# Optimization experiments

Hardware: AMD Instinct MI355X
Metric: run time of the kernel (lower is better)

## Reference

```python
import jax, jax.numpy as jnp
import numpy as np

B, N, D = 8, 4096, 256
H = 8
DH = D // H          # 32 per-head dim
M = 256              # number of random features
DEPTH = 4
HID = 4 * D          # mlp hidden
EPS = 1e-6


def layernorm(x, g, b):
    mu = jnp.mean(x, axis=-1, keepdims=True)
    var = jnp.mean(jnp.square(x - mu), axis=-1, keepdims=True)
    return (x - mu) * jax.lax.rsqrt(var + EPS) * g + b


def _phi(t, proj, is_query):
    # t: (B,H,N,DH), proj: (M,DH) -> (B,H,N,M) nonnegative softmax-kernel features
    nrm = DH ** -0.25
    td = t * nrm
    u = jnp.einsum('bhnd,md->bhnm', td, proj)
    diag = 0.5 * jnp.sum(td * td, axis=-1, keepdims=True)
    if is_query:
        mx = jnp.max(u, axis=-1, keepdims=True)
    else:
        mx = jnp.max(u, axis=(-2, -1), keepdims=True)
    return (jnp.exp(u - diag - mx) + 1e-4) / jnp.sqrt(jnp.asarray(M, t.dtype))


def performer_attn(h, Wqkv, Wproj, bproj, proj):
    # h: (B,N,D)
    qkv = h @ Wqkv                                   # (B,N,3D)
    q, k, v = jnp.split(qkv, 3, axis=-1)
    to_heads = lambda t: t.reshape(B, N, H, DH).transpose(0, 2, 1, 3)
    q, k, v = to_heads(q), to_heads(k), to_heads(v)  # (B,H,N,DH)
    qp = _phi(q, proj, True)                         # (B,H,N,M)
    kp = _phi(k, proj, False)                        # (B,H,N,M)
    kv = jnp.einsum('bhnm,bhnd->bhmd', kp, v)        # (B,H,M,DH) linear-time context
    z = 1.0 / (jnp.einsum('bhnm,bhm->bhn', qp, kp.sum(axis=2)) + 1e-6)
    out = jnp.einsum('bhnm,bhmd->bhnd', qp, kv) * z[..., None]
    out = out.transpose(0, 2, 1, 3).reshape(B, N, D)
    return out @ Wproj + bproj


def mlp(h, W1, b1, W2, b2):
    return jax.nn.gelu(h @ W1 + b1, approximate=False) @ W2 + b2


def setup_inputs() -> dict:
    key = jax.random.key(0)
    ks = jax.random.split(key, 10)
    inp = {
        'x': jax.random.normal(ks[0], (B, N, D), jnp.float32),
        'pos_emb': 0.02 * jax.random.normal(ks[1], (N, D), jnp.float32),
        'g1n': jnp.ones((D,), jnp.float32),
        'b1n': jnp.zeros((D,), jnp.float32),
        'g2n': jnp.ones((D,), jnp.float32),
        'b2n': jnp.zeros((D,), jnp.float32),
        'Wqkv': 0.02 * jax.random.normal(ks[2], (DEPTH, D, 3 * D), jnp.float32),
        'Wproj': 0.02 * jax.random.normal(ks[3], (DEPTH, D, D), jnp.float32),
        'bproj': jnp.zeros((DEPTH, D), jnp.float32),
        'W1': 0.02 * jax.random.normal(ks[4], (DEPTH, D, HID), jnp.float32),
        'b1m': jnp.zeros((DEPTH, HID), jnp.float32),
        'W2': 0.02 * jax.random.normal(ks[5], (DEPTH, HID, D), jnp.float32),
        'b2m': jnp.zeros((DEPTH, D), jnp.float32),
        'proj_mat': jax.random.normal(ks[6], (DEPTH, M, DH), jnp.float32),
    }
    return inp


def reference(x, pos_emb, g1n, b1n, g2n, b2n, Wqkv, Wproj, bproj, W1, b1m, W2, b2m, proj_mat):
    h = x + pos_emb[None]
    for l in range(DEPTH):  # small fixed depth
        h = h + performer_attn(layernorm(h, g1n, b1n), Wqkv[l], Wproj[l], bproj[l], proj_mat[l])
        h = h + mlp(layernorm(h, g2n, b2n), W1[l], b1m[l], W2[l], b2m[l])
    return h
```

## Files before the change

### kernel.cpp

```cpp
#include <hip/hip_runtime.h>
#include <hip/hip_bf16.h>
#include <math.h>

#define B 8
#define N 4096
#define D 256
#define H 8
#define DH 32
#define M 256
#define DEPTH 4
#define HID 1024
#define NRM 0.4204482076268573f

typedef __attribute__((ext_vector_type(8))) short short8;
typedef __attribute__((ext_vector_type(4))) float f32x4;

static __device__ __forceinline__ unsigned short f2bf(float f) {
    __hip_bfloat16 h = __float2bfloat16(f);
    return __builtin_bit_cast(unsigned short, h);
}
static __device__ __forceinline__ float bfu2f(unsigned short u) {
    unsigned int x = ((unsigned int)u) << 16;
    return __builtin_bit_cast(float, x);
}

__global__ void add_pos_kernel(const float* __restrict__ x, const float* __restrict__ pos,
                               float* __restrict__ h) {
    int i = blockIdx.x * 256 + threadIdx.x;
    int nd = i % (N * D);
    h[i] = x[i] + pos[nd];
}

__global__ void projbf_kernel(const float* __restrict__ in, unsigned short* __restrict__ out) {
    int i = blockIdx.x * 256 + threadIdx.x;
    out[i] = f2bf(in[i]);
}

__global__ __launch_bounds__(256) void wtrans_kernel(const float* __restrict__ in,
                                                     unsigned short* __restrict__ out,
                                                     int Kd, int Nd, int slim) {
    __shared__ float tl[32][33];
    int n0 = blockIdx.x * 32, k0 = blockIdx.y * 32;
    int t = threadIdx.x;
    int kk = t >> 3, c4 = (t & 7) * 4;
    float4 v = *reinterpret_cast<const float4*>(&in[(size_t)(k0 + kk) * Nd + n0 + c4]);
    tl[kk][c4 + 0] = v.x; tl[kk][c4 + 1] = v.y; tl[kk][c4 + 2] = v.z; tl[kk][c4 + 3] = v.w;
    __syncthreads();
    int nn = t >> 3, k4 = (t & 7) * 4;
    float sc = (n0 + nn < slim) ? NRM : 1.0f;
    ushort4 o;
    o.x = f2bf(tl[k4 + 0][nn] * sc); o.y = f2bf(tl[k4 + 1][nn] * sc);
    o.z = f2bf(tl[k4 + 2][nn] * sc); o.w = f2bf(tl[k4 + 3][nn] * sc);
    *reinterpret_cast<ushort4*>(&out[(size_t)(n0 + nn) * Kd + k0 + k4]) = o;
}

__global__ __launch_bounds__(256) void ln_kernel(const float* __restrict__ in,
                                                 const float* __restrict__ g,
                                                 const float* __restrict__ bb,
                                                 unsigned short* __restrict__ out) {
    int wave = threadIdx.x >> 6, lane = threadIdx.x & 63;
    long row = (long)blockIdx.x * 4 + wave;
    float4 v = reinterpret_cast<const float4*>(in + row * D)[lane];
    float s = v.x + v.y + v.z + v.w;
#pragma unroll
    for (int o = 32; o >= 1; o >>= 1) s += __shfl_xor(s, o);
    float mu = s * (1.0f / D);
    float d0 = v.x - mu, d1 = v.y - mu, d2 = v.z - mu, d3 = v.w - mu;
    float ss = d0 * d0 + d1 * d1 + d2 * d2 + d3 * d3;
#pragma unroll
    for (int o = 32; o >= 1; o >>= 1) ss += __shfl_xor(ss, o);
    float inv = rsqrtf(ss * (1.0f / D) + 1e-6f);
    float4 gv = reinterpret_cast<const float4*>(g)[lane];
    float4 bv = reinterpret_cast<const float4*>(bb)[lane];
    ushort4 o4;
    o4.x = f2bf(d0 * inv * gv.x + bv.x);
    o4.y = f2bf(d1 * inv * gv.y + bv.y);
    o4.z = f2bf(d2 * inv * gv.z + bv.z);
    o4.w = f2bf(d3 * inv * gv.w + bv.w);
    *reinterpret_cast<ushort4*>(&out[row * D + lane * 4]) = o4;
}

template <bool BIAS, bool GELU_ACT, bool RESID, bool OUT16>
__global__ __launch_bounds__(256) void mgemm_kernel(const unsigned short* __restrict__ A,
                                                    const unsigned short* __restrict__ Bt,
                                                    const float* __restrict__ bias,
                                                    float* __restrict__ C,
                                                    unsigned short* __restrict__ O16,
                                                    int K, int Nc) {
    __shared__ short Als[128][40];
    __shared__ short Bls[128][40];
    int t = threadIdx.x;
    int l = t & 63, w = t >> 6;
    int wr = w >> 1, wc = w & 1;
    int nwg = gridDim.x * gridDim.y;
    int bid = blockIdx.y * gridDim.x + blockIdx.x;
    int lgid = (bid & 7) * (nwg >> 3) + (bid >> 3);
    int bx = lgid % gridDim.x;
    int by = lgid / gridDim.x;
    long m0 = (long)by * 128;
    int n0 = bx * 128;
    int lr = l & 15;
    int lg = l >> 4;
    int kp8 = lg * 8;
    int srow = t >> 2, skoff = (t & 3) * 8;

    const unsigned short* Ap0 = &A[(size_t)(m0 + srow) * K + skoff];
    const unsigned short* Ap1 = Ap0 + (size_t)64 * K;
    const unsigned short* Bp0 = &Bt[(size_t)(n0 + srow) * K + skoff];
    const unsigned short* Bp1 = Bp0 + (size_t)64 * K;

    short8 ra0 = *reinterpret_cast<const short8*>(Ap0);
    short8 ra1 = *reinterpret_cast<const short8*>(Ap1);
    short8 rb0 = *reinterpret_cast<const short8*>(Bp0);
    short8 rb1 = *reinterpret_cast<const short8*>(Bp1);

    f32x4 acc[4][4];
#pragma unroll
    for (int i = 0; i < 4; i++)
#pragma unroll
        for (int j = 0; j < 4; j++) acc[i][j] = (f32x4){0.f, 0.f, 0.f, 0.f};

    for (int k0 = 0; k0 < K; k0 += 32) {
        *reinterpret_cast<short8*>(&Als[srow][skoff]) = ra0;
        *reinterpret_cast<short8*>(&Als[srow + 64][skoff]) = ra1;
        *reinterpret_cast<short8*>(&Bls[srow][skoff]) = rb0;
        *reinterpret_cast<short8*>(&Bls[srow + 64][skoff]) = rb1;
        __syncthreads();
        if (k0 + 32 < K) {
            ra0 = *reinterpret_cast<const short8*>(Ap0 + k0 + 32);
            ra1 = *reinterpret_cast<const short8*>(Ap1 + k0 + 32);
            rb0 = *reinterpret_cast<const short8*>(Bp0 + k0 + 32);
            rb1 = *reinterpret_cast<const short8*>(Bp1 + k0 + 32);
        }
        short8 a[4], b[4];
#pragma unroll
        for (int i = 0; i < 4; i++)
            a[i] = *reinterpret_cast<const short8*>(&Als[wr * 64 + i * 16 + lr][kp8]);
#pragma unroll
        for (int j = 0; j < 4; j++)
            b[j] = *reinterpret_cast<const short8*>(&Bls[wc * 64 + j * 16 + lr][kp8]);
#pragma unroll
        for (int i = 0; i < 4; i++)
#pragma unroll
            for (int j = 0; j < 4; j++)
                acc[i][j] = __builtin_amdgcn_mfma_f32_16x16x32_bf16(b[j], a[i], acc[i][j], 0, 0, 0);
        __syncthreads();
    }

    float4 bias4[4];
    if (BIAS) {
#pragma unroll
        for (int j = 0; j < 4; j++)
            bias4[j] = *reinterpret_cast<const float4*>(&bias[n0 + wc * 64 + j * 16 + lg * 4]);
    }
#pragma unroll
    for (int i = 0; i < 4; i++) {
        long grow = m0 + wr * 64 + i * 16 + lr;
#pragma unroll
        for (int j = 0; j < 4; j++) {
            int gcol = n0 + wc * 64 + j * 16 + lg * 4;
            f32x4 v = acc[i][j];
            if (BIAS) {
                v[0] += bias4[j].x; v[1] += bias4[j].y; v[2] += bias4[j].z; v[3] += bias4[j].w;
            }
            if (GELU_ACT) {
#pragma unroll
                for (int r = 0; r < 4; r++)
                    v[r] = 0.5f * v[r] * (1.0f + erff(v[r] * 0.70710678118654752f));
            }
            if (OUT16) {
                short4 o;
                o.x = (short)f2bf(v[0]); o.y = (short)f2bf(v[1]);
                o.z = (short)f2bf(v[2]); o.w = (short)f2bf(v[3]);
                *reinterpret_cast<short4*>(&O16[grow * Nc + gcol]) = o;
            } else if (RESID) {
                float4 c0 = *reinterpret_cast<const float4*>(&C[grow * Nc + gcol]);
                c0.x += v[0]; c0.y += v[1]; c0.z += v[2]; c0.w += v[3];
                *reinterpret_cast<float4*>(&C[grow * Nc + gcol]) = c0;
            } else {
                float4 c0 = {v[0], v[1], v[2], v[3]};
                *reinterpret_cast<float4*>(&C[grow * Nc + gcol]) = c0;
            }
        }
    }
}

__global__ __launch_bounds__(256) void mlp_fused_kernel(const unsigned short* __restrict__ ln16,
                                                        const unsigned short* __restrict__ w1T,
                                                        const unsigned short* __restrict__ w2T,
                                                        const float* __restrict__ b1,
                                                        const float* __restrict__ b2,
                                                        float* __restrict__ hres) {
    __shared__ __align__(16) unsigned short A_s[64][256];
    __shared__ __align__(16) unsigned short t1_s[64][128];
    int t = threadIdx.x;
    int l = t & 63, w = t >> 6;
    int lr = l & 15, lg = l >> 4;
    long m0 = (long)blockIdx.x * 64;
    int rsw = (lr & 7) << 3;

    {
        int r = t >> 2, c0 = (t & 3) * 64;
        const unsigned short* src = ln16 + (size_t)(m0 + r) * 256 + c0;
        int sw = (r & 7) << 3;
#pragma unroll
        for (int i = 0; i < 8; i++) {
            short8 v = *reinterpret_cast<const short8*>(src + i * 8);
            *reinterpret_cast<short8*>(&A_s[r][(c0 + i * 8) ^ sw]) = v;
        }
    }
    __syncthreads();

    f32x4 oacc[4][4];
#pragma unroll
    for (int i = 0; i < 4; i++)
#pragma unroll
        for (int j = 0; j < 4; j++) oacc[i][j] = (f32x4){0.f, 0.f, 0.f, 0.f};

    for (int ch = 0; ch < HID / 128; ch++) {
        f32x4 acc1[4][2];
#pragma unroll
        for (int mf = 0; mf < 4; mf++)
#pragma unroll
            for (int nh = 0; nh < 2; nh++) acc1[mf][nh] = (f32x4){0.f, 0.f, 0.f, 0.f};
#pragma unroll
        for (int ks = 0; ks < 8; ks++) {
#pragma unroll
            for (int nh = 0; nh < 2; nh++) {
                short8 wf = *reinterpret_cast<const short8*>(
                    &w1T[(size_t)(ch * 128 + w * 32 + nh * 16 + lr) * 256 + ks * 32 + lg * 8]);
#pragma unroll
                for (int mf = 0; mf < 4; mf++) {
                    short8 af = *reinterpret_cast<const short8*>(
                        &A_s[mf * 16 + lr][(ks * 32 + lg * 8) ^ rsw]);
                    acc1[mf][nh] = __builtin_amdgcn_mfma_f32_16x16x32_bf16(wf, af, acc1[mf][nh], 0, 0, 0);
                }
            }
        }
        __syncthreads();
#pragma unroll
        for (int nh = 0; nh < 2; nh++) {
            float4 b1v = *reinterpret_cast<const float4*>(&b1[ch * 128 + w * 32 + nh * 16 + lg * 4]);
#pragma unroll
            for (int mf = 0; mf < 4; mf++) {
                f32x4 v = acc1[mf][nh];
                v[0] += b1v.x; v[1] += b1v.y; v[2] += b1v.z; v[3] += b1v.w;
#pragma unroll
                for (int r = 0; r < 4; r++)
                    v[r] = 0.5f * v[r] * (1.0f + erff(v[r] * 0.70710678118654752f));
                short4 o;
                o.x = (short)f2bf(v[0]); o.y = (short)f2bf(v[1]);
                o.z = (short)f2bf(v[2]); o.w = (short)f2bf(v[3]);
                *reinterpret_cast<short4*>(&t1_s[mf * 16 + lr][(w * 32 + nh * 16 + lg * 4) ^ rsw]) = o;
            }
        }
        __syncthreads();
#pragma unroll
        for (int ks = 0; ks < 4; ks++) {
#pragma unroll
            for (int nf = 0; nf < 4; nf++) {
                short8 wf = *reinterpret_cast<const short8*>(
                    &w2T[(size_t)(w * 64 + nf * 16 + lr) * 1024 + ch * 128 + ks * 32 + lg * 8]);
#pragma unroll
                for (int mf = 0; mf < 4; mf++) {
                    short8 tf = *reinterpret_cast<const short8*>(
                        &t1_s[mf * 16 + lr][(ks * 32 + lg * 8) ^ rsw]);
                    oacc[mf][nf] = __builtin_amdgcn_mfma_f32_16x16x32_bf16(wf, tf, oacc[mf][nf], 0, 0, 0);
                }
            }
        }
    }

#pragma unroll
    for (int nf = 0; nf < 4; nf++) {
        float4 b2v = *reinterpret_cast<const float4*>(&b2[w * 64 + nf * 16 + lg * 4]);
#pragma unroll
        for (int mf = 0; mf < 4; mf++) {
            long grow = m0 + mf * 16 + lr;
            int gcol = w * 64 + nf * 16 + lg * 4;
            f32x4 v = oacc[mf][nf];
            float4 c0 = *reinterpret_cast<const float4*>(&hres[grow * 256 + gcol]);
            c0.x += v[0] + b2v.x; c0.y += v[1] + b2v.y;
            c0.z += v[2] + b2v.z; c0.w += v[3] + b2v.w;
            *reinterpret_cast<float4*>(&hres[grow * 256 + gcol]) = c0;
        }
    }
}

#define KV_P 16
#define KV_ROWS (N / KV_P)
#define PSZ 8484
__global__ __launch_bounds__(256) void kv_kernel(const unsigned short* __restrict__ qkv16,
                                                 const unsigned short* __restrict__ projbf,
                                                 float* __restrict__ kvp) {
    __shared__ __align__(16) unsigned short kp_s[256][64];
    __shared__ __align__(16) unsigned short vT_s[32][66];
    __shared__ float red[4];
    __shared__ float asumred[4][256];
    __shared__ float vred[256][4];
    int t = threadIdx.x;
    int l = t & 63, w = t >> 6;
    int lr = l & 15, lg = l >> 4;
    int bh = blockIdx.x, b = bh >> 3, h = bh & 7;
    int n0 = blockIdx.y * KV_ROWS;
    int rsw = (lr & 7) << 3;

    f32x4 kvacc[4][2];
#pragma unroll
    for (int mf = 0; mf < 4; mf++)
#pragma unroll
        for (int dd = 0; dd < 2; dd++) kvacc[mf][dd] = (f32x4){0.f, 0.f, 0.f, 0.f};
    float asum_p[16];
#pragma unroll
    for (int f = 0; f < 16; f++) asum_p[f] = 0.f;
    float4 vs4 = {0.f, 0.f, 0.f, 0.f};
    float Lm = -1e30f;

    for (int c = 0; c < KV_ROWS / 64; c++) {
        size_t kbase = ((size_t)(b * N) + n0 + c * 64 + w * 16 + lr) * 768 + 256 + h * 32 + lg * 8;
        short8 aq = *reinterpret_cast<const short8*>(qkv16 + kbase);
        float sq = 0.f;
#pragma unroll
        for (int e = 0; e < 8; e++) {
            float xx = bfu2f((unsigned short)aq[e]);
            sq += xx * xx;
        }
        sq += __shfl_xor(sq, 16);
        sq += __shfl_xor(sq, 32);
        f32x4 ua[16];
#pragma unroll
        for (int f = 0; f < 16; f++) {
            short8 bq = *reinterpret_cast<const short8*>(projbf + (f * 16 + lr) * 32 + lg * 8);
            ua[f] = __builtin_amdgcn_mfma_f32_16x16x32_bf16(aq, bq, (f32x4){0.f, 0.f, 0.f, 0.f}, 0, 0, 0);
        }
        float cm = -1e30f;
#pragma unroll
        for (int f = 0; f < 16; f++)
#pragma unroll
            for (int r = 0; r < 4; r++) cm = fmaxf(cm, ua[f][r]);
#pragma unroll
        for (int o = 1; o < 64; o <<= 1) cm = fmaxf(cm, __shfl_xor(cm, o));
        if (l == 0) red[w] = cm;
        __syncthreads();
        float bm = fmaxf(fmaxf(red[0], red[1]), fmaxf(red[2], red[3]));
        if (bm > Lm) {
            float sc = __expf(Lm - bm);
#pragma unroll
            for (int mf = 0; mf < 4; mf++)
#pragma unroll
                for (int dd = 0; dd < 2; dd++) {
                    kvacc[mf][dd][0] *= sc; kvacc[mf][dd][1] *= sc;
                    kvacc[mf][dd][2] *= sc; kvacc[mf][dd][3] *= sc;
                }
#pragma unroll
            for (int f = 0; f < 16; f++) asum_p[f] *= sc;
            Lm = bm;
        }
        float dgr[4];
#pragma unroll
        for (int r = 0; r < 4; r++) dgr[r] = 0.5f * __shfl(sq, lg * 4 + r);
        int cbase = (w * 16 + lg * 4) ^ rsw;
#pragma unroll
        for (int f = 0; f < 16; f++) {
            float p0 = __expf(ua[f][0] - dgr[0] - Lm);
            float p1 = __expf(ua[f][1] - dgr[1] - Lm);
            float p2 = __expf(ua[f][2] - dgr[2] - Lm);
            float p3 = __expf(ua[f][3] - dgr[3] - Lm);
            asum_p[f] += p0 + p1 + p2 + p3;
            short4 o;
            o.x = (short)f2bf(p0); o.y = (short)f2bf(p1);
            o.z = (short)f2bf(p2); o.w = (short)f2bf(p3);
            *reinterpret_cast<short4*>(&kp_s[f * 16 + lr][cbase]) = o;
        }
#pragma unroll
        for (int ii = 0; ii < 2; ii++) {
            int idx = t + ii * 256;
            int nn = idx >> 3, dz = (idx & 7) * 4;
            const unsigned short* vp =
                qkv16 + ((size_t)(b * N) + n0 + c * 64 + nn) * 768 + 512 + h * 32 + dz;
            short4 vv = *reinterpret_cast<const short4*>(vp);
            float v0 = bfu2f((unsigned short)vv.x), v1 = bfu2f((unsigned short)vv.y);
            float v2 = bfu2f((unsigned short)vv.z), v3 = bfu2f((unsigned short)vv.w);
            vs4.x += v0; vs4.y += v1; vs4.z += v2; vs4.w += v3;
            vT_s[dz + 0][nn] = (unsigned short)vv.x; vT_s[dz + 1][nn] = (unsigned short)vv.y;
            vT_s[dz + 2][nn] = (unsigned short)vv.z; vT_s[dz + 3][nn] = (unsigned short)vv.w;
        }
        __syncthreads();
#pragma unroll
        for (int ks = 0; ks < 2; ks++) {
            short8 bv0 = *reinterpret_cast<const short8*>(&vT_s[lr][ks * 32 + lg * 8]);
            short8 bv1 = *reinterpret_cast<const short8*>(&vT_s[16 + lr][ks * 32 + lg * 8]);
#pragma unroll
            for (int mf = 0; mf < 4; mf++) {
                short8 am = *reinterpret_cast<const short8*>(
                    &kp_s[w * 64 + mf * 16 + lr][(ks * 32 + lg * 8) ^ rsw]);
                kvacc[mf][0] = __builtin_amdgcn_mfma_f32_16x16x32_bf16(am, bv0, kvacc[mf][0], 0, 0, 0);
                kvacc[mf][1] = __builtin_amdgcn_mfma_f32_16x16x32_bf16(am, bv1, kvacc[mf][1], 0, 0, 0);
            }
        }
    }
#pragma unroll
    for (int f = 0; f < 16; f++) {
        asum_p[f] += __shfl_xor(asum_p[f], 16);
        asum_p[f] += __shfl_xor(asum_p[f], 32);
    }
    if (l < 16) {
#pragma unroll
        for (int f = 0; f < 16; f++) asumred[w][f * 16 + l] = asum_p[f];
    }
    vred[t][0] = vs4.x; vred[t][1] = vs4.y; vred[t][2] = vs4.z; vred[t][3] = vs4.w;
    __syncthreads();
    size_t base = ((size_t)bh * KV_P + blockIdx.y) * PSZ;
#pragma unroll
    for (int mf = 0; mf < 4; mf++)
#pragma unroll
        for (int dd = 0; dd < 2; dd++)
#pragma unroll
            for (int r = 0; r < 4; r++) {
                int m = w * 64 + mf * 16 + lg * 4 + r;
                int d = dd * 16 + lr;
                kvp[base + m * 32 + d] = kvacc[mf][dd][r];
            }
    {
        float s = asumred[0][t] + asumred[1][t] + asumred[2][t] + asumred[3][t];
        kvp[base + 8192 + t] = s;
    }
    if (t < 32) {
        int f4g = t >> 2, cc = t & 3;
        float s = 0.f;
#pragma unroll
        for (int g = 0; g < 32; g++) s += vred[g * 8 + f4g][cc];
        kvp[base + 8448 + t] = s;
    }
    if (t == 0) kvp[base + 8480] = Lm;
}

__global__ __launch_bounds__(256) void kv_combine_kernel(const float* __restrict__ kvp,
                                                         unsigned short* __restrict__ kvTb,
                                                         float* __restrict__ ksumf) {
    __shared__ float vst[32];
    int t = threadIdx.x;
    int bh = blockIdx.x >> 2, mq = blockIdx.x & 3;
    size_t base0 = (size_t)bh * KV_P * PSZ;
    float Lp[KV_P];
    float gm = -1e30f;
#pragma unroll
    for (int p = 0; p < KV_P; p++) {
        Lp[p] = kvp[base0 + p * PSZ + 8480];
        gm = fmaxf(gm, Lp[p]);
    }
    if (t < 32) {
        float s = 0.f;
#pragma unroll
        for (int p = 0; p < KV_P; p++) s += kvp[base0 + p * PSZ + 8448 + t];
        vst[t] = s;
    }
    __syncthreads();
    int m = mq * 64 + (t >> 2);
    int d0 = (t & 3) * 8;
    float4 av0 = {0.f, 0.f, 0.f, 0.f}, av1 = {0.f, 0.f, 0.f, 0.f};
    float S = 0.f;
#pragma unroll
    for (int p = 0; p < KV_P; p++) {
        float e = __expf(Lp[p] - gm);
        size_t pb = base0 + p * PSZ;
        float4 a = *reinterpret_cast<const float4*>(&kvp[pb + m * 32 + d0]);
        float4 bq = *reinterpret_cast<const float4*>(&kvp[pb + m * 32 + d0 + 4]);
        av0.x += e * a.x; av0.y += e * a.y; av0.z += e * a.z; av0.w += e * a.w;
        av1.x += e * bq.x; av1.y += e * bq.y; av1.z += e * bq.z; av1.w += e * bq.w;
        if ((t & 3) == 0) S += e * kvp[pb + 8192 + m];
    }
    float o[8];
    o[0] = av0.x; o[1] = av0.y; o[2] = av0.z; o[3] = av0.w;
    o[4] = av1.x; o[5] = av1.y; o[6] = av1.z; o[7] = av1.w;
#pragma unroll
    for (int j = 0; j < 8; j++) {
        float v = (o[j] + 1e-4f * vst[d0 + j]) * 0.0625f;
        kvTb[((size_t)bh * 32 + d0 + j) * 256 + m] = f2bf(v);
    }
    if ((t & 3) == 0) ksumf[bh * 256 + m] = (S + 1e-4f * (float)N) * 0.0625f;
}

#define ATT_TILES 8
__global__ __launch_bounds__(256) void attn_kernel(const unsigned short* __restrict__ qkv16,
                                                   const unsigned short* __restrict__ projbf,
                                                   const unsigned short* __restrict__ kvTb,
                                                   const float* __restrict__ ksumf,
                                                   unsigned short* __restrict__ attn16) {
    __shared__ __align__(16) unsigned short qp_s[64 * 256];
    int t = threadIdx.x;
    int l = t & 63, w = t >> 6;
    int lr = l & 15, lg = l >> 4;
    int bh = blockIdx.x, b = bh >> 3, h = bh & 7;
    int swz = (lr & 7) << 3;
    int row = w * 16 + lr;

    const unsigned short* kvb = kvTb + (size_t)bh * 32 * 256;
    short8 kva0[8], kva1[8];
#pragma unroll
    for (int k0 = 0; k0 < 8; k0++) {
        kva0[k0] = *reinterpret_cast<const short8*>(kvb + (size_t)lr * 256 + k0 * 32 + lg * 8);
        kva1[k0] = *reinterpret_cast<const short8*>(kvb + (size_t)(16 + lr) * 256 + k0 * 32 + lg * 8);
    }

    int tile0 = blockIdx.y * ATT_TILES;
    size_t qstep = (size_t)64 * 768;
    size_t qbase = ((size_t)(b * N) + tile0 * 64 + w * 16 + lr) * 768 + h * 32 + lg * 8;
    short8 qf = *reinterpret_cast<const short8*>(qkv16 + qbase);

    for (int tl = 0; tl < ATT_TILES; tl++) {
        short8 qfn = qf;
        if (tl < ATT_TILES - 1)
            qfn = *reinterpret_cast<const short8*>(qkv16 + qbase + (size_t)(tl + 1) * qstep);

        float sq = 0.f;
#pragma unroll
        for (int e = 0; e < 8; e++) {
            float xx = bfu2f((unsigned short)qf[e]);
            sq += xx * xx;
        }
        sq += __shfl_xor(sq, 16);
        sq += __shfl_xor(sq, 32);
        float dg = 0.5f * sq;

        f32x4 ua[16];
#pragma unroll
        for (int f = 0; f < 16; f++) {
            short8 bq = *reinterpret_cast<const short8*>(projbf + (f * 16 + lr) * 32 + lg * 8);
            ua[f] = __builtin_amdgcn_mfma_f32_16x16x32_bf16(bq, qf, (f32x4){0.f, 0.f, 0.f, 0.f}, 0, 0, 0);
        }

        float mx = -1e30f;
#pragma unroll
        for (int f = 0; f < 16; f++)
#pragma unroll
            for (int r = 0; r < 4; r++) mx = fmaxf(mx, ua[f][r]);
        mx = fmaxf(mx, __shfl_xor(mx, 16));
        mx = fmaxf(mx, __shfl_xor(mx, 32));

        float zs = 0.f;
#pragma unroll
        for (int f = 0; f < 16; f++) {
            float4 ks4 = *reinterpret_cast<const float4*>(&ksumf[bh * 256 + f * 16 + lg * 4]);
            float p0 = (__expf(ua[f][0] - dg - mx) + 1e-4f) * 0.0625f;
            float p1 = (__expf(ua[f][1] - dg - mx) + 1e-4f) * 0.0625f;
            float p2 = (__expf(ua[f][2] - dg - mx) + 1e-4f) * 0.0625f;
            float p3 = (__expf(ua[f][3] - dg - mx) + 1e-4f) * 0.0625f;
            zs += p0 * ks4.x + p1 * ks4.y + p2 * ks4.z + p3 * ks4.w;
            short4 o;
            o.x = (short)f2bf(p0); o.y = (short)f2bf(p1);
            o.z = (short)f2bf(p2); o.w = (short)f2bf(p3);
            *reinterpret_cast<short4*>(&qp_s[row * 256 + ((f * 16 + lg * 4) ^ swz)]) = o;
        }
        zs += __shfl_xor(zs, 16);
        zs += __shfl_xor(zs, 32);
        float zf = 1.0f / (zs + 1e-6f);

        f32x4 oacc[2];
        oacc[0] = (f32x4){0.f, 0.f, 0.f, 0.f};
        oacc[1] = (f32x4){0.f, 0.f, 0.f, 0.f};
#pragma unroll
        for (int k0 = 0; k0 < 8; k0++) {
            short8 qpf = *reinterpret_cast<const short8*>(
                &qp_s[row * 256 + ((k0 * 32 + lg * 8) ^ swz)]);
            oacc[0] = __builtin_amdgcn_mfma_f32_16x16x32_bf16(kva0[k0], qpf, oacc[0], 0, 0, 0);
            oacc[1] = __builtin_amdgcn_mfma_f32_16x16x32_bf16(kva1[k0], qpf, oacc[1], 0, 0, 0);
        }
        size_t orow = ((size_t)(b * N) + (tile0 + tl) * 64 + w * 16 + lr) * 256 + h * 32;
#pragma unroll
        for (int dd = 0; dd < 2; dd++) {
            short4 o;
            o.x = (short)f2bf(oacc[dd][0] * zf);
            o.y = (short)f2bf(oacc[dd][1] * zf);
            o.z = (short)f2bf(oacc[dd][2] * zf);
            o.w = (short)f2bf(oacc[dd][3] * zf);
            *reinterpret_cast<short4*>(&attn16[orow + dd * 16 + lg * 4]) = o;
        }
        qf = qfn;
    }
}

extern "C" void kernel_launch(void* const* d_in, const int* in_sizes, int n_in,
                              void* d_out, int out_size, void* d_ws, size_t ws_size,
                              hipStream_t stream) {
    const float* x = (const float*)d_in[0];
    const float* pos = (const float*)d_in[1];
    const float* g1 = (const float*)d_in[2];
    const float* b1 = (const float*)d_in[3];
    const float* g2 = (const float*)d_in[4];
    const float* b2 = (const float*)d_in[5];
    const float* Wqkv = (const float*)d_in[6];
    const float* Wproj = (const float*)d_in[7];
    const float* bproj = (const float*)d_in[8];
    const float* W1 = (const float*)d_in[9];
    const float* b1m = (const float*)d_in[10];
    const float* W2 = (const float*)d_in[11];
    const float* b2m = (const float*)d_in[12];
    const float* projm = (const float*)d_in[13];

    float* h = (float*)d_out;
    char* p = (char*)d_ws;
    auto alloc = [&](size_t bytes) { char* r = p; p += (bytes + 255) & ~(size_t)255; return r; };
    unsigned short* wbf    = (unsigned short*)alloc((size_t)DEPTH * 786432 * 2);
    unsigned short* projb  = (unsigned short*)alloc((size_t)DEPTH * M * DH * 2);
    unsigned short* ln16   = (unsigned short*)alloc((size_t)B * N * D * 2);
    unsigned short* qkv16  = (unsigned short*)alloc((size_t)B * N * 3 * D * 2);
    unsigned short* attn16 = (unsigned short*)alloc((size_t)B * N * D * 2);
    float* kvp             = (float*)alloc((size_t)64 * KV_P * PSZ * 4);
    unsigned short* kvTb   = (unsigned short*)alloc((size_t)64 * 32 * 256 * 2);
    float* ksumf           = (float*)alloc((size_t)64 * 256 * 4);

    for (int l = 0; l < DEPTH; l++) {
        size_t lb = (size_t)l * 786432;
        wtrans_kernel<<<dim3(768 / 32, 256 / 32), 256, 0, stream>>>(
            Wqkv + (size_t)l * D * 3 * D, wbf + lb + 0, 256, 768, 512);
        wtrans_kernel<<<dim3(256 / 32, 256 / 32), 256, 0, stream>>>(
            Wproj + (size_t)l * D * D, wbf + lb + 196608, 256, 256, 0);
        wtrans_kernel<<<dim3(1024 / 32, 256 / 32), 256, 0, stream>>>(
            W1 + (size_t)l * D * HID, wbf + lb + 262144, 256, 1024, 0);
        wtrans_kernel<<<dim3(256 / 32, 1024 / 32), 256, 0, stream>>>(
            W2 + (size_t)l * HID * D, wbf + lb + 524288, 1024, 256, 0);
    }
    projbf_kernel<<<DEPTH * M * DH / 256, 256, 0, stream>>>(projm, projb);

    add_pos_kernel<<<B * N * D / 256, 256, 0, stream>>>(x, pos, h);

    for (int l = 0; l < DEPTH; l++) {
        size_t lb = (size_t)l * 786432;
        const unsigned short* wqT = wbf + lb + 0;
        const unsigned short* wpT = wbf + lb + 196608;
        const unsigned short* w1T = wbf + lb + 262144;
        const unsigned short* w2T = wbf + lb + 524288;
        const float* bp = bproj + (size_t)l * D;
        const float* b1l = b1m + (size_t)l * HID;
        const float* b2l = b2m + (size_t)l * D;
        const unsigned short* prb = projb + (size_t)l * M * DH;

        ln_kernel<<<B * N / 4, 256, 0, stream>>>(h, g1, b1, ln16);
        mgemm_kernel<false, false, false, true><<<dim3(768 / 128, B * N / 128), 256, 0, stream>>>(
            ln16, wqT, nullptr, nullptr, qkv16, 256, 768);
        kv_kernel<<<dim3(B * H, KV_P), 256, 0, stream>>>(qkv16, prb, kvp);
        kv_combine_kernel<<<B * H * 4, 256, 0, stream>>>(kvp, kvTb, ksumf);
        attn_kernel<<<dim3(B * H, (N / 64) / ATT_TILES), 256, 0, stream>>>(
            qkv16, prb, kvTb, ksumf, attn16);
        mgemm_kernel<true, false, true, false><<<dim3(256 / 128, B * N / 128), 256, 0, stream>>>(
            attn16, wpT, bp, h, nullptr, 256, 256);
        ln_kernel<<<B * N / 4, 256, 0, stream>>>(h, g2, b2, ln16);
        mlp_fused_kernel<<<B * N / 64, 256, 0, stream>>>(ln16, w1T, w2T, b1l, b2l, h);
    }
}
```

Before: 1.076 ms.

## Assign each wave its own 16 rows in fused MLP, drop shared A tile and barriers

Restructures the fused MLP kernel so each wave owns 16 token rows across the full hidden and output dims, instead of the four waves splitting columns of a shared 64-row tile. Activation fragments are loaded straight from global memory into registers, which removes the A_s shared buffer and both __syncthreads per chunk, since t1_s is now private to each wave. The trade-off is that every wave now loads the whole W1 and W2 chunks itself, so weight traffic per block goes up roughly fourfold. Register pressure also rises with 16 output accumulators plus 8 cached A fragments.

```diff
diff --git a/kernel.cpp b/kernel.cpp
--- a/kernel.cpp
+++ b/kernel.cpp
@@ -191,99 +191,70 @@
                                                         const float* __restrict__ b1,
                                                         const float* __restrict__ b2,
                                                         float* __restrict__ hres) {
-    __shared__ __align__(16) unsigned short A_s[64][256];
     __shared__ __align__(16) unsigned short t1_s[64][128];
     int t = threadIdx.x;
     int l = t & 63, w = t >> 6;
     int lr = l & 15, lg = l >> 4;
     long m0 = (long)blockIdx.x * 64;
+    int row = w * 16 + lr;
     int rsw = (lr & 7) << 3;
 
-    {
-        int r = t >> 2, c0 = (t & 3) * 64;
-        const unsigned short* src = ln16 + (size_t)(m0 + r) * 256 + c0;
-        int sw = (r & 7) << 3;
-#pragma unroll
-        for (int i = 0; i < 8; i++) {
-            short8 v = *reinterpret_cast<const short8*>(src + i * 8);
-            *reinterpret_cast<short8*>(&A_s[r][(c0 + i * 8) ^ sw]) = v;
-        }
-    }
-    __syncthreads();
-
-    f32x4 oacc[4][4];
-#pragma unroll
-    for (int i = 0; i < 4; i++)
-#pragma unroll
-        for (int j = 0; j < 4; j++) oacc[i][j] = (f32x4){0.f, 0.f, 0.f, 0.f};
+    const unsigned short* arow = ln16 + (size_t)(m0 + row) * 256;
+    short8 af[8];
+#pragma unroll
+    for (int ks = 0; ks < 8; ks++)
+        af[ks] = *reinterpret_cast<const short8*>(arow + ks * 32 + lg * 8);
+
+    f32x4 oacc[16];
+#pragma unroll
+    for (int nf = 0; nf < 16; nf++) oacc[nf] = (f32x4){0.f, 0.f, 0.f, 0.f};
 
     for (int ch = 0; ch < HID / 128; ch++) {
-        f32x4 acc1[4][2];
-#pragma unroll
-        for (int mf = 0; mf < 4; mf++)
-#pragma unroll
-            for (int nh = 0; nh < 2; nh++) acc1[mf][nh] = (f32x4){0.f, 0.f, 0.f, 0.f};
-#pragma unroll
-        for (int ks = 0; ks < 8; ks++) {
-#pragma unroll
-            for (int nh = 0; nh < 2; nh++) {
+        f32x4 acc1[8];
+#pragma unroll
+        for (int f = 0; f < 8; f++) acc1[f] = (f32x4){0.f, 0.f, 0.f, 0.f};
+#pragma unroll
+        for (int f = 0; f < 8; f++) {
+            const unsigned short* w1r = w1T + (size_t)(ch * 128 + f * 16 + lr) * 256 + lg * 8;
+#pragma unroll
+            for (int ks = 0; ks < 8; ks++) {
+                short8 wf = *reinterpret_cast<const short8*>(w1r + ks * 32);
+                acc1[f] = __builtin_amdgcn_mfma_f32_16x16x32_bf16(wf, af[ks], acc1[f], 0, 0, 0);
+            }
+        }
+#pragma unroll
+        for (int f = 0; f < 8; f++) {
+            float4 b1v = *reinterpret_cast<const float4*>(&b1[ch * 128 + f * 16 + lg * 4]);
+            f32x4 v = acc1[f];
+            v[0] += b1v.x; v[1] += b1v.y; v[2] += b1v.z; v[3] += b1v.w;
+#pragma unroll
+            for (int r = 0; r < 4; r++)
+                v[r] = 0.5f * v[r] * (1.0f + erff(v[r] * 0.70710678118654752f));
+            short4 o;
+            o.x = (short)f2bf(v[0]); o.y = (short)f2bf(v[1]);
+            o.z = (short)f2bf(v[2]); o.w = (short)f2bf(v[3]);
+            *reinterpret_cast<short4*>(&t1_s[row][(f * 16 + lg * 4) ^ rsw]) = o;
+        }
+#pragma unroll
+        for (int k0 = 0; k0 < 4; k0++) {
+            short8 tf = *reinterpret_cast<const short8*>(&t1_s[row][(k0 * 32 + lg * 8) ^ rsw]);
+#pragma unroll
+            for (int nf = 0; nf < 16; nf++) {
                 short8 wf = *reinterpret_cast<const short8*>(
-                    &w1T[(size_t)(ch * 128 + w * 32 + nh * 16 + lr) * 256 + ks * 32 + lg * 8]);
-#pragma unroll
-                for (int mf = 0; mf < 4; mf++) {
-                    short8 af = *reinterpret_cast<const short8*>(
-                        &A_s[mf * 16 + lr][(ks * 32 + lg * 8) ^ rsw]);
-                    acc1[mf][nh] = __builtin_amdgcn_mfma_f32_16x16x32_bf16(wf, af, acc1[mf][nh], 0, 0, 0);
-                }
+                    &w2T[(size_t)(nf * 16 + lr) * 1024 + ch * 128 + k0 * 32 + lg * 8]);
+                oacc[nf] = __builtin_amdgcn_mfma_f32_16x16x32_bf16(wf, tf, oacc[nf], 0, 0, 0);
             }
         }
-        __syncthreads();
-#pragma unroll
-        for (int nh = 0; nh < 2; nh++) {
-            float4 b1v = *reinterpret_cast<const float4*>(&b1[ch * 128 + w * 32 + nh * 16 + lg * 4]);
-#pragma unroll
-            for (int mf = 0; mf < 4; mf++) {
-                f32x4 v = acc1[mf][nh];
-                v[0] += b1v.x; v[1] += b1v.y; v[2] += b1v.z; v[3] += b1v.w;
-#pragma unroll
-                for (int r = 0; r < 4; r++)
-                    v[r] = 0.5f * v[r] * (1.0f + erff(v[r] * 0.70710678118654752f));
-                short4 o;
-                o.x = (short)f2bf(v[0]); o.y = (short)f2bf(v[1]);
-                o.z = (short)f2bf(v[2]); o.w = (short)f2bf(v[3]);
-                *reinterpret_cast<short4*>(&t1_s[mf * 16 + lr][(w * 32 + nh * 16 + lg * 4) ^ rsw]) = o;
-            }
-        }
-        __syncthreads();
-#pragma unroll
-        for (int ks = 0; ks < 4; ks++) {
-#pragma unroll
-            for (int nf = 0; nf < 4; nf++) {
-                short8 wf = *reinterpret_cast<const short8*>(
-                    &w2T[(size_t)(w * 64 + nf * 16 + lr) * 1024 + ch * 128 + ks * 32 + lg * 8]);
-#pragma unroll
-                for (int mf = 0; mf < 4; mf++) {
-                    short8 tf = *reinterpret_cast<const short8*>(
-                        &t1_s[mf * 16 + lr][(ks * 32 + lg * 8) ^ rsw]);
-                    oacc[mf][nf] = __builtin_amdgcn_mfma_f32_16x16x32_bf16(wf, tf, oacc[mf][nf], 0, 0, 0);
-                }
-            }
-        }
-    }
-
-#pragma unroll
-    for (int nf = 0; nf < 4; nf++) {
-        float4 b2v = *reinterpret_cast<const float4*>(&b2[w * 64 + nf * 16 + lg * 4]);
-#pragma unroll
-        for (int mf = 0; mf < 4; mf++) {
-            long grow = m0 + mf * 16 + lr;
-            int gcol = w * 64 + nf * 16 + lg * 4;
-            f32x4 v = oacc[mf][nf];
-            float4 c0 = *reinterpret_cast<const float4*>(&hres[grow * 256 + gcol]);
-            c0.x += v[0] + b2v.x; c0.y += v[1] + b2v.y;
-            c0.z += v[2] + b2v.z; c0.w += v[3] + b2v.w;
-            *reinterpret_cast<float4*>(&hres[grow * 256 + gcol]) = c0;
-        }
+    }
+
+    float* hrow = &hres[(size_t)(m0 + row) * 256];
+#pragma unroll
+    for (int nf = 0; nf < 16; nf++) {
+        float4 b2v = *reinterpret_cast<const float4*>(&b2[nf * 16 + lg * 4]);
+        float4 c0 = *reinterpret_cast<const float4*>(hrow + nf * 16 + lg * 4);
+        c0.x += oacc[nf][0] + b2v.x; c0.y += oacc[nf][1] + b2v.y;
+        c0.z += oacc[nf][2] + b2v.z; c0.w += oacc[nf][3] + b2v.w;
+        *reinterpret_cast<float4*>(hrow + nf * 16 + lg * 4) = c0;
     }
 }
 
```

Measured after the change: 1.866 ms. 1.73x slower.
